# Optimization experiments

Measured on AMD Instinct MI355X. Metric: run time of the kernel, lower is better.

## Reference

```python
import jax, jax.numpy as jnp
import numpy as np

# Graph constants: 3 leaves -> 3 hidden layers of 128 nodes (with recurrent
# self-loops) -> 3 output nodes, over a 256x512 spatial substrate.
N_LEAVES, HID, N_OUT, SH, SW = 3, 128, 3, 256, 512


def setup_inputs() -> dict:
    key = jax.random.key(0)
    ks = jax.random.split(key, 9)
    inv = 1.0 / np.sqrt(HID)
    return {
        "x_in": jax.random.normal(ks[0], (N_LEAVES, SH, SW), jnp.float32),
        "W_in": jax.random.normal(ks[1], (HID, N_LEAVES), jnp.float32) * 0.5,
        "W_h": jax.random.normal(ks[2], (2, HID, HID), jnp.float32) * inv,
        "r_rec": jax.random.normal(ks[3], (3, HID), jnp.float32) * 0.1,
        "resp": 1.0 + 0.1 * jax.random.normal(ks[4], (3, HID), jnp.float32),
        "bias": 0.1 * jax.random.normal(ks[5], (3, HID), jnp.float32),
        "W_out": jax.random.normal(ks[6], (N_OUT, HID), jnp.float32) * inv,
        "resp_out": jnp.ones((N_OUT,), jnp.float32),
        "b_out": 0.1 * jax.random.normal(ks[7], (N_OUT,), jnp.float32),
        "n_iters": 2,
    }


def reference(x_in, W_in, W_h, r_rec, resp, bias, W_out, resp_out, b_out, n_iters):
    # One timestep of the recursive DAG evaluation, batched per layer.
    # Node math: act = tanh(response * (sum_j w_j * x_j) + bias), where the
    # self-loop child contributes r * activs_previous (zeros at t=0).
    def step(H_prev, _):
        pre0 = jnp.einsum('hc,cij->hij', W_in, x_in) + r_rec[0][:, None, None] * H_prev[0]
        h0 = jnp.tanh(resp[0][:, None, None] * pre0 + bias[0][:, None, None])
        pre1 = jnp.einsum('hk,kij->hij', W_h[0], h0) + r_rec[1][:, None, None] * H_prev[1]
        h1 = jnp.tanh(resp[1][:, None, None] * pre1 + bias[1][:, None, None])
        pre2 = jnp.einsum('hk,kij->hij', W_h[1], h1) + r_rec[2][:, None, None] * H_prev[2]
        h2 = jnp.tanh(resp[2][:, None, None] * pre2 + bias[2][:, None, None])
        out = jnp.tanh(resp_out[:, None, None] * jnp.einsum('oh,hij->oij', W_out, h2)
                       + b_out[:, None, None])
        return jnp.stack([h0, h1, h2]), out

    H0 = jnp.zeros((3, HID, x_in.shape[1], x_in.shape[2]), x_in.dtype)
    _, outs = jax.lax.scan(step, H0, None, length=n_iters)
    return outs[-1]  # [N_OUT, SH, SW]
```

## Files before the change

### kernel.cpp

```cpp
#include <hip/hip_runtime.h>
#include <hip/hip_bf16.h>

#define HID   128
#define PBLK  128
#define NPIX  (256*512)
#define L2E2  2.88539008177792681f

typedef __attribute__((ext_vector_type(8))) short bf16x8;
typedef __attribute__((ext_vector_type(4))) float f32x4;

#if __has_builtin(__builtin_amdgcn_exp2f)
__device__ inline float fexp2(float x) { return __builtin_amdgcn_exp2f(x); }
#else
__device__ inline float fexp2(float x) { return exp2f(x); }
#endif

__device__ inline unsigned pack2(float a, float b) {
    __hip_bfloat16 lo = __float2bfloat16(a);
    __hip_bfloat16 hi = __float2bfloat16(b);
    unsigned short ul = *reinterpret_cast<unsigned short*>(&lo);
    unsigned short uh = *reinterpret_cast<unsigned short*>(&hi);
    return (unsigned)ul | ((unsigned)uh << 16);
}
__device__ inline float ulo(unsigned u) { union { unsigned u; float f; } v; v.u = u << 16;        return v.f; }
__device__ inline float uhi(unsigned u) { union { unsigned u; float f; } v; v.u = u & 0xffff0000u; return v.f; }

__device__ inline float actf(float u) {
    float e = fexp2(u);
    return 1.0f - 2.0f * __builtin_amdgcn_rcpf(e + 1.0f);
}

__device__ inline bf16x8 bc(uint4 v) { return __builtin_bit_cast(bf16x8, v); }

__device__ __forceinline__ uint2 quadact(f32x4 a, uint2 rec, float4 bet) {
    float v0 = actf(fmaf(bet.x, ulo(rec.x), a[0]));
    float v1 = actf(fmaf(bet.y, uhi(rec.x), a[1]));
    float v2 = actf(fmaf(bet.z, ulo(rec.y), a[2]));
    float v3 = actf(fmaf(bet.w, uhi(rec.y), a[3]));
    return make_uint2(pack2(v0, v1), pack2(v2, v3));
}

__global__ __launch_bounds__(256) void prep_weights(
    const float* __restrict__ W_h, const float* __restrict__ W_out,
    const float* __restrict__ resp, const float* __restrict__ resp_out,
    unsigned short* __restrict__ ws)
{
    int c = blockIdx.x * 256 + threadIdx.x;
    if (c < 4096) {
        int l = c & 63, kb = (c >> 6) & 3, aidx = (c >> 8) & 1, rt2 = (c >> 9) & 3, lay = (c >> 11) & 1;
        int row = rt2 * 32 + aidx * 16 + (l & 15);
        int k   = kb * 32 + (l >> 4) * 8;
        float al = L2E2 * resp[(lay + 1) * HID + row];
        const float* src = W_h + (lay * HID + row) * HID + k;
        float4 f0 = *(const float4*)src, f1 = *(const float4*)(src + 4);
        uint4 v;
        v.x = pack2(al * f0.x, al * f0.y); v.y = pack2(al * f0.z, al * f0.w);
        v.z = pack2(al * f1.x, al * f1.y); v.w = pack2(al * f1.z, al * f1.w);
        *(uint4*)(ws + (size_t)c * 8) = v;
    } else if (c < 4352) {
        int c2 = c - 4096, l = c2 & 63, kb = c2 >> 6;
        int row = l & 15, k = kb * 32 + (l >> 4) * 8;
        uint4 v = {0u, 0u, 0u, 0u};
        if (row < 3) {
            float al = L2E2 * resp_out[row];
            const float* src = W_out + row * HID + k;
            float4 f0 = *(const float4*)src, f1 = *(const float4*)(src + 4);
            v.x = pack2(al * f0.x, al * f0.y); v.y = pack2(al * f0.z, al * f0.w);
            v.z = pack2(al * f1.x, al * f1.y); v.w = pack2(al * f1.z, al * f1.w);
        }
        *(uint4*)(ws + 32768 + (size_t)c2 * 8) = v;
    }
}

__global__ __launch_bounds__(1024) void fused_net(
    const float* __restrict__ x_in,
    const float* __restrict__ W_in,
    const float* __restrict__ r_rec,
    const float* __restrict__ resp,
    const float* __restrict__ bias,
    const float* __restrict__ b_out,
    const int*   __restrict__ n_iters_p,
    const unsigned short* __restrict__ wsw,
    float* __restrict__ out)
{
    __shared__ __align__(16) uint4 Wh_lds[4096];
    __shared__ __align__(16) unsigned short P0s[8 * 4 * 64 * 8];
    __shared__ __align__(16) unsigned short P1s[8 * 4 * 64 * 8];
    __shared__ float4 Winp_s[HID];
    __shared__ float  beta_s[3 * HID];
    __shared__ float  gamma_s[2 * HID];
    __shared__ float  gammao_s[16];
    __shared__ float  xs[3 * PBLK];

    const int t = threadIdx.x;
    const int w = t >> 6, l = t & 63;
    const int lr = l & 15, lg = l >> 4;
    const int rt2 = w >> 2;
    const int ct  = w & 3;
    const int pixbase = (int)blockIdx.x * PBLK;
    const int niters = *n_iters_p;
    const uint4* wsU = (const uint4*)wsw;

    #pragma unroll
    for (int i = 0; i < 4; ++i) Wh_lds[t + i * 1024] = wsU[t + i * 1024];
    if (t < 3 * HID) beta_s[t] = L2E2 * resp[t] * r_rec[t];
    if (t < 2 * HID) gamma_s[t] = L2E2 * bias[HID + t];
    if (t < HID) {
        float a = L2E2 * resp[t];
        float4 pv;
        pv.x = a * W_in[t * 3 + 0];
        pv.y = a * W_in[t * 3 + 1];
        pv.z = a * W_in[t * 3 + 2];
        pv.w = L2E2 * bias[t];
        Winp_s[t] = pv;
    }
    if (t < 16) gammao_s[t] = (t < 3) ? L2E2 * b_out[t] : 0.0f;
    if (t < 3 * PBLK) xs[t] = x_in[(t >> 7) * NPIX + pixbase + (t & 127)];
    __syncthreads();

    const int p0 = t & 127, hb2 = t >> 7;
    const float x0 = xs[p0], x1 = xs[128 + p0], x2 = xs[256 + p0];

    unsigned rec0[8];
    uint2 rec1_00{0,0}, rec1_01{0,0}, rec1_10{0,0}, rec1_11{0,0};
    uint2 rec2_00{0,0}, rec2_01{0,0}, rec2_10{0,0}, rec2_11{0,0};
    #pragma unroll
    for (int i = 0; i < 8; ++i) rec0[i] = 0u;

    const bf16x8* P0c = (const bf16x8*)P0s;
    const bf16x8* P1c = (const bf16x8*)P1s;
    const uint4* AP0 = Wh_lds + rt2 * 512 + l;
    const uint4* AP1 = Wh_lds + (4 + rt2) * 512 + l;

    const float4 bt1A = *(const float4*)(beta_s + HID + rt2 * 32 + lg * 4);
    const float4 bt1B = *(const float4*)(beta_s + HID + rt2 * 32 + 16 + lg * 4);
    const float4 bt2A = *(const float4*)(beta_s + 2 * HID + rt2 * 32 + lg * 4);
    const float4 bt2B = *(const float4*)(beta_s + 2 * HID + rt2 * 32 + 16 + lg * 4);
    const float4 gm1A = *(const float4*)(gamma_s + rt2 * 32 + lg * 4);
    const float4 gm1B = *(const float4*)(gamma_s + rt2 * 32 + 16 + lg * 4);
    const float4 gm2A = *(const float4*)(gamma_s + HID + rt2 * 32 + lg * 4);
    const float4 gm2B = *(const float4*)(gamma_s + HID + rt2 * 32 + 16 + lg * 4);

    const int wr00 = (((ct * 2 + 0) * 4 + rt2) * 64 + (0 + (lg >> 1)) * 16 + lr) * 8 + (lg & 1) * 4;
    const int wr01 = (((ct * 2 + 1) * 4 + rt2) * 64 + (0 + (lg >> 1)) * 16 + lr) * 8 + (lg & 1) * 4;
    const int wr10 = (((ct * 2 + 0) * 4 + rt2) * 64 + (2 + (lg >> 1)) * 16 + lr) * 8 + (lg & 1) * 4;
    const int wr11 = (((ct * 2 + 1) * 4 + rt2) * 64 + (2 + (lg >> 1)) * 16 + lr) * 8 + (lg & 1) * 4;

    for (int it = 0; it < niters; ++it) {
        #pragma unroll
        for (int s = 0; s < 2; ++s) {
            uint4 ov;
            #pragma unroll
            for (int q = 0; q < 4; ++q) {
                int c = s * 8 + q * 2, h = hb2 * 16 + c;
                float4 wp0 = Winp_s[h], wp1 = Winp_s[h + 1];
                float bet0 = beta_s[h], bet1 = beta_s[h + 1];
                unsigned rp = rec0[s * 4 + q];
                float c1a = fmaf(wp0.x, x0, fmaf(wp0.y, x1, fmaf(wp0.z, x2, wp0.w)));
                float c1b = fmaf(wp1.x, x0, fmaf(wp1.y, x1, fmaf(wp1.z, x2, wp1.w)));
                float v0 = actf(fmaf(bet0, ulo(rp), c1a));
                float v1 = actf(fmaf(bet1, uhi(rp), c1b));
                unsigned pk = pack2(v0, v1);
                rec0[s * 4 + q] = pk;
                if (q == 0) ov.x = pk; else if (q == 1) ov.y = pk;
                else if (q == 2) ov.z = pk; else ov.w = pk;
            }
            int h8 = hb2 * 16 + s * 8;
            int chunk = ((p0 >> 4) * 4 + (h8 >> 5)) * 64 + ((h8 >> 3) & 3) * 16 + (p0 & 15);
            *(uint4*)(P0s + chunk * 8) = ov;
        }
        __syncthreads();

        {
            const bf16x8* SB = P0c + (ct * 8) * 64 + l;
            f32x4 acc0{gm1A.x, gm1A.y, gm1A.z, gm1A.w};
            f32x4 acc1 = acc0;
            f32x4 acc2{gm1B.x, gm1B.y, gm1B.z, gm1B.w};
            f32x4 acc3 = acc2;
            #pragma unroll
            for (int kb = 0; kb < 4; ++kb) {
                bf16x8 a0 = bc(AP0[kb * 64]);
                bf16x8 a1 = bc(AP0[(4 + kb) * 64]);
                bf16x8 b0 = SB[kb * 64];
                bf16x8 b1 = SB[(4 + kb) * 64];
                acc0 = __builtin_amdgcn_mfma_f32_16x16x32_bf16(a0, b0, acc0, 0, 0, 0);
                acc1 = __builtin_amdgcn_mfma_f32_16x16x32_bf16(a0, b1, acc1, 0, 0, 0);
                acc2 = __builtin_amdgcn_mfma_f32_16x16x32_bf16(a1, b0, acc2, 0, 0, 0);
                acc3 = __builtin_amdgcn_mfma_f32_16x16x32_bf16(a1, b1, acc3, 0, 0, 0);
            }
            rec1_00 = quadact(acc0, rec1_00, bt1A);
            rec1_01 = quadact(acc1, rec1_01, bt1A);
            rec1_10 = quadact(acc2, rec1_10, bt1B);
            rec1_11 = quadact(acc3, rec1_11, bt1B);
            *(uint2*)(P1s + wr00) = rec1_00;
            *(uint2*)(P1s + wr01) = rec1_01;
            *(uint2*)(P1s + wr10) = rec1_10;
            *(uint2*)(P1s + wr11) = rec1_11;
        }
        __syncthreads();

        {
            const bool last = (it == niters - 1);
            const bf16x8* SB = P1c + (ct * 8) * 64 + l;
            f32x4 acc0{gm2A.x, gm2A.y, gm2A.z, gm2A.w};
            f32x4 acc1 = acc0;
            f32x4 acc2{gm2B.x, gm2B.y, gm2B.z, gm2B.w};
            f32x4 acc3 = acc2;
            #pragma unroll
            for (int kb = 0; kb < 4; ++kb) {
                bf16x8 a0 = bc(AP1[kb * 64]);
                bf16x8 a1 = bc(AP1[(4 + kb) * 64]);
                bf16x8 b0 = SB[kb * 64];
                bf16x8 b1 = SB[(4 + kb) * 64];
                acc0 = __builtin_amdgcn_mfma_f32_16x16x32_bf16(a0, b0, acc0, 0, 0, 0);
                acc1 = __builtin_amdgcn_mfma_f32_16x16x32_bf16(a0, b1, acc1, 0, 0, 0);
                acc2 = __builtin_amdgcn_mfma_f32_16x16x32_bf16(a1, b0, acc2, 0, 0, 0);
                acc3 = __builtin_amdgcn_mfma_f32_16x16x32_bf16(a1, b1, acc3, 0, 0, 0);
            }
            rec2_00 = quadact(acc0, rec2_00, bt2A);
            rec2_01 = quadact(acc1, rec2_01, bt2A);
            rec2_10 = quadact(acc2, rec2_10, bt2B);
            rec2_11 = quadact(acc3, rec2_11, bt2B);
            if (last) {
                *(uint2*)(P0s + wr00) = rec2_00;
                *(uint2*)(P0s + wr01) = rec2_01;
                *(uint2*)(P0s + wr10) = rec2_10;
                *(uint2*)(P0s + wr11) = rec2_11;
            }
        }
    }
    __syncthreads();

    if (w < 8) {
        float4 go = *(const float4*)(gammao_s + lg * 4);
        f32x4 oacc{go.x, go.y, go.z, go.w};
        const uint4* OA = wsU + 4096 + l;
        const bf16x8* OB = P0c + (w * 4) * 64 + l;
        oacc = __builtin_amdgcn_mfma_f32_16x16x32_bf16(bc(OA[0 * 64]), OB[0 * 64], oacc, 0, 0, 0);
        oacc = __builtin_amdgcn_mfma_f32_16x16x32_bf16(bc(OA[1 * 64]), OB[1 * 64], oacc, 0, 0, 0);
        oacc = __builtin_amdgcn_mfma_f32_16x16x32_bf16(bc(OA[2 * 64]), OB[2 * 64], oacc, 0, 0, 0);
        oacc = __builtin_amdgcn_mfma_f32_16x16x32_bf16(bc(OA[3 * 64]), OB[3 * 64], oacc, 0, 0, 0);
        int p = pixbase + w * 16 + lr;
        if (lg == 0) {
            out[0 * NPIX + p] = actf(oacc[0]);
            out[1 * NPIX + p] = actf(oacc[1]);
            out[2 * NPIX + p] = actf(oacc[2]);
        }
    }
}

extern "C" void kernel_launch(void* const* d_in, const int* in_sizes, int n_in,
                              void* d_out, int out_size, void* d_ws, size_t ws_size,
                              hipStream_t stream) {
    const float* x_in     = (const float*)d_in[0];
    const float* W_in     = (const float*)d_in[1];
    const float* W_h      = (const float*)d_in[2];
    const float* r_rec    = (const float*)d_in[3];
    const float* resp     = (const float*)d_in[4];
    const float* bias     = (const float*)d_in[5];
    const float* W_out    = (const float*)d_in[6];
    const float* resp_out = (const float*)d_in[7];
    const float* b_out    = (const float*)d_in[8];
    const int*   n_iters  = (const int*)d_in[9];
    float* out = (float*)d_out;
    unsigned short* ws = (unsigned short*)d_ws;

    prep_weights<<<17, 256, 0, stream>>>(W_h, W_out, resp, resp_out, ws);
    fused_net<<<NPIX / PBLK, 1024, 0, stream>>>(x_in, W_in, r_rec, resp, bias,
                                                b_out, n_iters, ws, out);
}
```

Baseline: 54.24 us.

## Split pixel block into two halves and software-pipeline layers across them

The 128-pixel block is split into two 64-pixel halves with separate LDS planes. Layer GEMMs for one half are interleaved with the layer-0 elementwise work or the other layer's GEMM for the other half, so MFMA work overlaps VALU/transcendental work between barriers. This doubles activation LDS buffers and adds more complex phase scheduling and extra barriers, in exchange for fewer idle pipeline stalls per barrier phase.

Result: slower. 65.26 us (+20.3%).

```diff
diff --git a/kernel.cpp b/kernel.cpp
--- a/kernel.cpp
+++ b/kernel.cpp
@@ -2,7 +2,6 @@
 #include <hip/hip_bf16.h>
 
 #define HID   128
-#define PBLK  128
 #define NPIX  (256*512)
 #define L2E2  2.88539008177792681f
 
@@ -72,6 +71,48 @@
     }
 }
 
+#define L0_PHASE(PS, xv0, xv1, xv2, recarr)                                        \
+    {                                                                              \
+        uint4 ov;                                                                  \
+        _Pragma("unroll")                                                          \
+        for (int q = 0; q < 4; ++q) {                                              \
+            int h = hb2 * 8 + q * 2;                                               \
+            float4 wp0 = Winp_s[h], wp1 = Winp_s[h + 1];                           \
+            float bet0 = beta_s[h], bet1 = beta_s[h + 1];                          \
+            unsigned rp = recarr[q];                                               \
+            float c1a = fmaf(wp0.x, xv0, fmaf(wp0.y, xv1, fmaf(wp0.z, xv2, wp0.w))); \
+            float c1b = fmaf(wp1.x, xv0, fmaf(wp1.y, xv1, fmaf(wp1.z, xv2, wp1.w))); \
+            float v0 = actf(fmaf(bet0, ulo(rp), c1a));                             \
+            float v1 = actf(fmaf(bet1, uhi(rp), c1b));                             \
+            unsigned pk = pack2(v0, v1);                                           \
+            recarr[q] = pk;                                                        \
+            if (q == 0) ov.x = pk; else if (q == 1) ov.y = pk;                     \
+            else if (q == 2) ov.z = pk; else ov.w = pk;                            \
+        }                                                                          \
+        *(uint4*)((PS) + l0chunk * 8) = ov;                                        \
+    }
+
+#define GEMM_ISSUE(SRC, AP, gm0, gm1, a0n, a1n)                                    \
+    f32x4 a0n{gm0.x, gm0.y, gm0.z, gm0.w};                                         \
+    f32x4 a1n{gm1.x, gm1.y, gm1.z, gm1.w};                                         \
+    {                                                                              \
+        const bf16x8* SBp = (const bf16x8*)(SRC) + (ctq * 4) * 64 + l;             \
+        _Pragma("unroll")                                                          \
+        for (int kb = 0; kb < 4; ++kb) {                                           \
+            bf16x8 bb = SBp[kb * 64];                                              \
+            a0n = __builtin_amdgcn_mfma_f32_16x16x32_bf16(bc((AP)[kb * 64]), bb, a0n, 0, 0, 0); \
+            a1n = __builtin_amdgcn_mfma_f32_16x16x32_bf16(bc((AP)[(4 + kb) * 64]), bb, a1n, 0, 0, 0); \
+        }                                                                          \
+    }
+
+#define GEMM_EPI(a0n, a1n, btm0, btm1, recm0, recm1, DST, dowrite)                 \
+    recm0 = quadact(a0n, recm0, btm0);                                             \
+    recm1 = quadact(a1n, recm1, btm1);                                             \
+    if (dowrite) {                                                                 \
+        *(uint2*)((DST) + wrm0) = recm0;                                           \
+        *(uint2*)((DST) + wrm1) = recm1;                                           \
+    }
+
 __global__ __launch_bounds__(1024) void fused_net(
     const float* __restrict__ x_in,
     const float* __restrict__ W_in,
@@ -84,20 +125,22 @@
     float* __restrict__ out)
 {
     __shared__ __align__(16) uint4 Wh_lds[4096];
-    __shared__ __align__(16) unsigned short P0s[8 * 4 * 64 * 8];
-    __shared__ __align__(16) unsigned short P1s[8 * 4 * 64 * 8];
+    __shared__ __align__(16) unsigned short PA0s[8192];
+    __shared__ __align__(16) unsigned short PA1s[8192];
+    __shared__ __align__(16) unsigned short PB0s[8192];
+    __shared__ __align__(16) unsigned short PB1s[8192];
     __shared__ float4 Winp_s[HID];
     __shared__ float  beta_s[3 * HID];
     __shared__ float  gamma_s[2 * HID];
     __shared__ float  gammao_s[16];
-    __shared__ float  xs[3 * PBLK];
+    __shared__ float  xs[3 * 128];
 
     const int t = threadIdx.x;
     const int w = t >> 6, l = t & 63;
     const int lr = l & 15, lg = l >> 4;
     const int rt2 = w >> 2;
-    const int ct  = w & 3;
-    const int pixbase = (int)blockIdx.x * PBLK;
+    const int ctq = w & 3;
+    const int pixbase = (int)blockIdx.x * 128;
     const int niters = *n_iters_p;
     const uint4* wsU = (const uint4*)wsw;
 
@@ -115,132 +158,88 @@
         Winp_s[t] = pv;
     }
     if (t < 16) gammao_s[t] = (t < 3) ? L2E2 * b_out[t] : 0.0f;
-    if (t < 3 * PBLK) xs[t] = x_in[(t >> 7) * NPIX + pixbase + (t & 127)];
-    __syncthreads();
-
-    const int p0 = t & 127, hb2 = t >> 7;
-    const float x0 = xs[p0], x1 = xs[128 + p0], x2 = xs[256 + p0];
-
-    unsigned rec0[8];
-    uint2 rec1_00{0,0}, rec1_01{0,0}, rec1_10{0,0}, rec1_11{0,0};
-    uint2 rec2_00{0,0}, rec2_01{0,0}, rec2_10{0,0}, rec2_11{0,0};
+    if (t < 3 * 128) xs[t] = x_in[(t >> 7) * NPIX + pixbase + (t & 127)];
+    __syncthreads();
+
+    const int p0 = t & 63, hb2 = t >> 6;
+    const int l0chunk = ((p0 >> 4) * 4 + (hb2 >> 2)) * 64 + (hb2 & 3) * 16 + (p0 & 15);
+    const float xa0 = xs[p0],      xa1 = xs[128 + p0],      xa2 = xs[256 + p0];
+    const float xb0 = xs[64 + p0], xb1 = xs[192 + p0],      xb2 = xs[320 + p0];
+
+    unsigned rec0a[4], rec0b[4];
     #pragma unroll
-    for (int i = 0; i < 8; ++i) rec0[i] = 0u;
-
-    const bf16x8* P0c = (const bf16x8*)P0s;
-    const bf16x8* P1c = (const bf16x8*)P1s;
+    for (int i = 0; i < 4; ++i) { rec0a[i] = 0u; rec0b[i] = 0u; }
+    uint2 rec1A0{0,0}, rec1A1{0,0}, rec1B0{0,0}, rec1B1{0,0};
+    uint2 rec2A0{0,0}, rec2A1{0,0}, rec2B0{0,0}, rec2B1{0,0};
+
     const uint4* AP0 = Wh_lds + rt2 * 512 + l;
     const uint4* AP1 = Wh_lds + (4 + rt2) * 512 + l;
 
-    const float4 bt1A = *(const float4*)(beta_s + HID + rt2 * 32 + lg * 4);
-    const float4 bt1B = *(const float4*)(beta_s + HID + rt2 * 32 + 16 + lg * 4);
-    const float4 bt2A = *(const float4*)(beta_s + 2 * HID + rt2 * 32 + lg * 4);
-    const float4 bt2B = *(const float4*)(beta_s + 2 * HID + rt2 * 32 + 16 + lg * 4);
-    const float4 gm1A = *(const float4*)(gamma_s + rt2 * 32 + lg * 4);
-    const float4 gm1B = *(const float4*)(gamma_s + rt2 * 32 + 16 + lg * 4);
-    const float4 gm2A = *(const float4*)(gamma_s + HID + rt2 * 32 + lg * 4);
-    const float4 gm2B = *(const float4*)(gamma_s + HID + rt2 * 32 + 16 + lg * 4);
-
-    const int wr00 = (((ct * 2 + 0) * 4 + rt2) * 64 + (0 + (lg >> 1)) * 16 + lr) * 8 + (lg & 1) * 4;
-    const int wr01 = (((ct * 2 + 1) * 4 + rt2) * 64 + (0 + (lg >> 1)) * 16 + lr) * 8 + (lg & 1) * 4;
-    const int wr10 = (((ct * 2 + 0) * 4 + rt2) * 64 + (2 + (lg >> 1)) * 16 + lr) * 8 + (lg & 1) * 4;
-    const int wr11 = (((ct * 2 + 1) * 4 + rt2) * 64 + (2 + (lg >> 1)) * 16 + lr) * 8 + (lg & 1) * 4;
+    const float4 b1m0 = *(const float4*)(beta_s + HID + rt2 * 32 + lg * 4);
+    const float4 b1m1 = *(const float4*)(beta_s + HID + rt2 * 32 + 16 + lg * 4);
+    const float4 b2m0 = *(const float4*)(beta_s + 2 * HID + rt2 * 32 + lg * 4);
+    const float4 b2m1 = *(const float4*)(beta_s + 2 * HID + rt2 * 32 + 16 + lg * 4);
+    const float4 g1m0 = *(const float4*)(gamma_s + rt2 * 32 + lg * 4);
+    const float4 g1m1 = *(const float4*)(gamma_s + rt2 * 32 + 16 + lg * 4);
+    const float4 g2m0 = *(const float4*)(gamma_s + HID + rt2 * 32 + lg * 4);
+    const float4 g2m1 = *(const float4*)(gamma_s + HID + rt2 * 32 + 16 + lg * 4);
+
+    const int wrm0 = ((ctq * 4 + rt2) * 64 + (0 + (lg >> 1)) * 16 + lr) * 8 + (lg & 1) * 4;
+    const int wrm1 = ((ctq * 4 + rt2) * 64 + (2 + (lg >> 1)) * 16 + lr) * 8 + (lg & 1) * 4;
+
+    L0_PHASE(PA0s, xa0, xa1, xa2, rec0a);
+    __syncthreads();
+
+    {
+        GEMM_ISSUE(PA0s, AP0, g1m0, g1m1, accA0, accA1);
+        L0_PHASE(PB0s, xb0, xb1, xb2, rec0b);
+        GEMM_EPI(accA0, accA1, b1m0, b1m1, rec1A0, rec1A1, PA1s, true);
+    }
+    __syncthreads();
 
     for (int it = 0; it < niters; ++it) {
-        #pragma unroll
-        for (int s = 0; s < 2; ++s) {
-            uint4 ov;
-            #pragma unroll
-            for (int q = 0; q < 4; ++q) {
-                int c = s * 8 + q * 2, h = hb2 * 16 + c;
-                float4 wp0 = Winp_s[h], wp1 = Winp_s[h + 1];
-                float bet0 = beta_s[h], bet1 = beta_s[h + 1];
-                unsigned rp = rec0[s * 4 + q];
-                float c1a = fmaf(wp0.x, x0, fmaf(wp0.y, x1, fmaf(wp0.z, x2, wp0.w)));
-                float c1b = fmaf(wp1.x, x0, fmaf(wp1.y, x1, fmaf(wp1.z, x2, wp1.w)));
-                float v0 = actf(fmaf(bet0, ulo(rp), c1a));
-                float v1 = actf(fmaf(bet1, uhi(rp), c1b));
-                unsigned pk = pack2(v0, v1);
-                rec0[s * 4 + q] = pk;
-                if (q == 0) ov.x = pk; else if (q == 1) ov.y = pk;
-                else if (q == 2) ov.z = pk; else ov.w = pk;
+        const bool last = (it == niters - 1);
+        {
+            GEMM_ISSUE(PA1s, AP1, g2m0, g2m1, accA0, accA1);
+            GEMM_ISSUE(PB0s, AP0, g1m0, g1m1, accB0, accB1);
+            GEMM_EPI(accA0, accA1, b2m0, b2m1, rec2A0, rec2A1, PA0s, last);
+            GEMM_EPI(accB0, accB1, b1m0, b1m1, rec1B0, rec1B1, PB1s, true);
+        }
+        __syncthreads();
+        if (!last) {
+            {
+                GEMM_ISSUE(PB1s, AP1, g2m0, g2m1, accB0, accB1);
+                L0_PHASE(PA0s, xa0, xa1, xa2, rec0a);
+                GEMM_EPI(accB0, accB1, b2m0, b2m1, rec2B0, rec2B1, PB0s, false);
             }
-            int h8 = hb2 * 16 + s * 8;
-            int chunk = ((p0 >> 4) * 4 + (h8 >> 5)) * 64 + ((h8 >> 3) & 3) * 16 + (p0 & 15);
-            *(uint4*)(P0s + chunk * 8) = ov;
-        }
-        __syncthreads();
-
-        {
-            const bf16x8* SB = P0c + (ct * 8) * 64 + l;
-            f32x4 acc0{gm1A.x, gm1A.y, gm1A.z, gm1A.w};
-            f32x4 acc1 = acc0;
-            f32x4 acc2{gm1B.x, gm1B.y, gm1B.z, gm1B.w};
-            f32x4 acc3 = acc2;
-            #pragma unroll
-            for (int kb = 0; kb < 4; ++kb) {
-                bf16x8 a0 = bc(AP0[kb * 64]);
-                bf16x8 a1 = bc(AP0[(4 + kb) * 64]);
-                bf16x8 b0 = SB[kb * 64];
-                bf16x8 b1 = SB[(4 + kb) * 64];
-                acc0 = __builtin_amdgcn_mfma_f32_16x16x32_bf16(a0, b0, acc0, 0, 0, 0);
-                acc1 = __builtin_amdgcn_mfma_f32_16x16x32_bf16(a0, b1, acc1, 0, 0, 0);
-                acc2 = __builtin_amdgcn_mfma_f32_16x16x32_bf16(a1, b0, acc2, 0, 0, 0);
-                acc3 = __builtin_amdgcn_mfma_f32_16x16x32_bf16(a1, b1, acc3, 0, 0, 0);
+            __syncthreads();
+            {
+                GEMM_ISSUE(PA0s, AP0, g1m0, g1m1, accA0, accA1);
+                L0_PHASE(PB0s, xb0, xb1, xb2, rec0b);
+                GEMM_EPI(accA0, accA1, b1m0, b1m1, rec1A0, rec1A1, PA1s, true);
             }
-            rec1_00 = quadact(acc0, rec1_00, bt1A);
-            rec1_01 = quadact(acc1, rec1_01, bt1A);
-            rec1_10 = quadact(acc2, rec1_10, bt1B);
-            rec1_11 = quadact(acc3, rec1_11, bt1B);
-            *(uint2*)(P1s + wr00) = rec1_00;
-            *(uint2*)(P1s + wr01) = rec1_01;
-            *(uint2*)(P1s + wr10) = rec1_10;
-            *(uint2*)(P1s + wr11) = rec1_11;
-        }
-        __syncthreads();
-
-        {
-            const bool last = (it == niters - 1);
-            const bf16x8* SB = P1c + (ct * 8) * 64 + l;
-            f32x4 acc0{gm2A.x, gm2A.y, gm2A.z, gm2A.w};
-            f32x4 acc1 = acc0;
-            f32x4 acc2{gm2B.x, gm2B.y, gm2B.z, gm2B.w};
-            f32x4 acc3 = acc2;
-            #pragma unroll
-            for (int kb = 0; kb < 4; ++kb) {
-                bf16x8 a0 = bc(AP1[kb * 64]);
-                bf16x8 a1 = bc(AP1[(4 + kb) * 64]);
-                bf16x8 b0 = SB[kb * 64];
-                bf16x8 b1 = SB[(4 + kb) * 64];
-                acc0 = __builtin_amdgcn_mfma_f32_16x16x32_bf16(a0, b0, acc0, 0, 0, 0);
-                acc1 = __builtin_amdgcn_mfma_f32_16x16x32_bf16(a0, b1, acc1, 0, 0, 0);
-                acc2 = __builtin_amdgcn_mfma_f32_16x16x32_bf16(a1, b0, acc2, 0, 0, 0);
-                acc3 = __builtin_amdgcn_mfma_f32_16x16x32_bf16(a1, b1, acc3, 0, 0, 0);
-            }
-            rec2_00 = quadact(acc0, rec2_00, bt2A);
-            rec2_01 = quadact(acc1, rec2_01, bt2A);
-            rec2_10 = quadact(acc2, rec2_10, bt2B);
-            rec2_11 = quadact(acc3, rec2_11, bt2B);
-            if (last) {
-                *(uint2*)(P0s + wr00) = rec2_00;
-                *(uint2*)(P0s + wr01) = rec2_01;
-                *(uint2*)(P0s + wr10) = rec2_10;
-                *(uint2*)(P0s + wr11) = rec2_11;
-            }
-        }
+            __syncthreads();
+        }
+    }
+
+    {
+        GEMM_ISSUE(PB1s, AP1, g2m0, g2m1, accB0, accB1);
+        GEMM_EPI(accB0, accB1, b2m0, b2m1, rec2B0, rec2B1, PB0s, true);
     }
     __syncthreads();
 
     if (w < 8) {
+        const int half = w >> 2, g = w & 3;
+        const unsigned short* plane = half ? PB0s : PA0s;
         float4 go = *(const float4*)(gammao_s + lg * 4);
         f32x4 oacc{go.x, go.y, go.z, go.w};
         const uint4* OA = wsU + 4096 + l;
-        const bf16x8* OB = P0c + (w * 4) * 64 + l;
+        const bf16x8* OB = (const bf16x8*)plane + (g * 4) * 64 + l;
         oacc = __builtin_amdgcn_mfma_f32_16x16x32_bf16(bc(OA[0 * 64]), OB[0 * 64], oacc, 0, 0, 0);
         oacc = __builtin_amdgcn_mfma_f32_16x16x32_bf16(bc(OA[1 * 64]), OB[1 * 64], oacc, 0, 0, 0);
         oacc = __builtin_amdgcn_mfma_f32_16x16x32_bf16(bc(OA[2 * 64]), OB[2 * 64], oacc, 0, 0, 0);
         oacc = __builtin_amdgcn_mfma_f32_16x16x32_bf16(bc(OA[3 * 64]), OB[3 * 64], oacc, 0, 0, 0);
-        int p = pixbase + w * 16 + lr;
+        int p = pixbase + half * 64 + g * 16 + lr;
         if (lg == 0) {
             out[0 * NPIX + p] = actf(oacc[0]);
             out[1 * NPIX + p] = actf(oacc[1]);
@@ -266,6 +265,6 @@
     unsigned short* ws = (unsigned short*)d_ws;
 
     prep_weights<<<17, 256, 0, stream>>>(W_h, W_out, resp, resp_out, ws);
-    fused_net<<<NPIX / PBLK, 1024, 0, stream>>>(x_in, W_in, r_rec, resp, bias,
-                                                b_out, n_iters, ws, out);
-}
+    fused_net<<<NPIX / 128, 1024, 0, stream>>>(x_in, W_in, r_rec, resp, bias,
+                                               b_out, n_iters, ws, out);
+}
```
